# Optimization experiments

Measured on AMD Instinct MI355X. Metric: run time of the kernel, lower is better.

## Reference

```python
import jax, jax.numpy as jnp
import numpy as np

D_MODEL = 512
N_LAYERS = 4
VOCAB = 256
SEQ = 2048
BATCH = 8
EPS = 1e-5


def _ln(x, g, b):
    mu = jnp.mean(x, axis=-1, keepdims=True)
    var = jnp.mean(jnp.square(x - mu), axis=-1, keepdims=True)
    return (x - mu) * jax.lax.rsqrt(var + EPS) * g + b


def setup_inputs() -> dict:
    key = jax.random.key(0)
    ks = jax.random.split(key, 16)
    d, dff = D_MODEL, 4 * D_MODEL
    s = 0.02
    inp = {
        "tokens": jax.random.randint(ks[0], (BATCH, SEQ), 0, VOCAB, dtype=jnp.int64),
        "emb": jax.random.normal(ks[1], (VOCAB, d), jnp.float32) * s,
        "W_upd": jax.random.normal(ks[2], (d, d), jnp.float32) * s,
        "b_upd": jnp.zeros((d,), jnp.float32),
        "W_f": jax.random.normal(ks[3], (d, d), jnp.float32) * s,
        "b_f": jnp.zeros((d,), jnp.float32),
        "decay_param": jnp.zeros((1,), jnp.float32),
        "norm_g": jnp.ones((d,), jnp.float32),
        "norm_b": jnp.zeros((d,), jnp.float32),
        "cms_ln_g": jnp.ones((N_LAYERS, d), jnp.float32),
        "cms_ln_b": jnp.zeros((N_LAYERS, d), jnp.float32),
        "cms_W1": jax.random.normal(ks[4], (N_LAYERS, d, dff), jnp.float32) * s,
        "cms_b1": jnp.zeros((N_LAYERS, dff), jnp.float32),
        "cms_W2": jax.random.normal(ks[5], (N_LAYERS, dff, d), jnp.float32) * s,
        "cms_b2": jnp.zeros((N_LAYERS, d), jnp.float32),
        "head_W": jax.random.normal(ks[6], (d, VOCAB), jnp.float32) * s,
        "head_b": jnp.zeros((VOCAB,), jnp.float32),
    }
    return inp


def _fast_memory(x, mask, W_upd, b_upd, W_f, b_f, decay_param):
    # x: (B,S,d), mask: (B,S) float
    decay = jax.nn.sigmoid(decay_param[0])
    u = jnp.einsum("bsd,de->bse", x, W_upd) + b_upd  # precompute updates
    u_t = jnp.swapaxes(u, 0, 1)                        # (S,B,d)
    m_t = jnp.swapaxes(mask, 0, 1)[..., None]          # (S,B,1)

    def step(mem, inp):
        u_i, msk = inp
        new = decay * mem + u_i
        mem = msk * new + (1.0 - msk) * mem
        return mem, mem

    mem0 = jnp.zeros((x.shape[0], x.shape[2]), x.dtype)
    _, mems = jax.lax.scan(step, mem0, (u_t, m_t))     # (S,B,d)
    mems = jnp.swapaxes(mems, 0, 1)                    # (B,S,d)
    return jnp.einsum("bsd,de->bse", mems, W_f) + b_f


def reference(tokens, emb, W_upd, b_upd, W_f, b_f, decay_param, norm_g, norm_b,
              cms_ln_g, cms_ln_b, cms_W1, cms_b1, cms_W2, cms_b2, head_W, head_b):
    mask = (tokens != 0).astype(emb.dtype)
    x = emb[tokens]                                    # (B,S,d)
    x = x + _fast_memory(x, mask, W_upd, b_upd, W_f, b_f, decay_param)
    x = _ln(x, norm_g, norm_b)
    for i in range(N_LAYERS):
        h = _ln(x, cms_ln_g[i], cms_ln_b[i])
        h = jax.nn.gelu(jnp.einsum("bsd,df->bsf", h, cms_W1[i]) + cms_b1[i], approximate=False)
        h = jnp.einsum("bsf,fd->bsd", h, cms_W2[i]) + cms_b2[i]
        x = x + h
    return jnp.einsum("bsd,dv->bsv", x, head_W) + head_b
```

## Files before the change

### kernel.cpp

```cpp
#include <hip/hip_runtime.h>
#include <hip/hip_bf16.h>
#include <math.h>

#define D_MODEL 512
#define N_LAYERS 4
#define SEQ 2048
#define BATCH 8
#define M_TOT (BATCH * SEQ)
#define DFF 2048
#define HEAD_V 256
#define SC 32
#define NC (SEQ / SC)

typedef __hip_bfloat16 bf16;
typedef __bf16 bf16x8 __attribute__((ext_vector_type(8)));
typedef float f32x4 __attribute__((ext_vector_type(4)));

__device__ __forceinline__ unsigned short bfbits(float x) {
    bf16 h = __float2bfloat16(x);
    return *(unsigned short*)&h;
}
__device__ __forceinline__ unsigned int pk(float a, float b) {
    return (unsigned int)bfbits(a) | ((unsigned int)bfbits(b) << 16);
}

__device__ __forceinline__ float gelu_f(float x) {
    float t2 = 1.5957691216f * (x + 0.044715f * x * x * x);
    float e = __expf(t2);
    return x - x * __builtin_amdgcn_rcpf(e + 1.0f);
}

__global__ void convT_kernel(const float* __restrict__ W, bf16* __restrict__ WT,
                             int R, int C, size_t wstride, size_t tstride) {
    W += (size_t)blockIdx.z * wstride;
    WT += (size_t)blockIdx.z * tstride;
    __shared__ float t[32][33];
    int r0 = blockIdx.x * 32, c0 = blockIdx.y * 32;
    int tx = threadIdx.x, ty = threadIdx.y;
    #pragma unroll
    for (int i = 0; i < 32; i += 8)
        t[ty + i][tx] = W[(size_t)(r0 + ty + i) * C + c0 + tx];
    __syncthreads();
    #pragma unroll
    for (int i = 0; i < 32; i += 8)
        WT[(size_t)(c0 + ty + i) * R + r0 + tx] = __float2bfloat16(t[tx][ty + i]);
}

__global__ void embed_kernel(const int* __restrict__ tokens,
                             const float* __restrict__ emb,
                             float* __restrict__ xf, bf16* __restrict__ xb) {
    int row = blockIdx.x, t = threadIdx.x;
    int tok = tokens[row];
    float4 v = ((const float4*)(emb + (size_t)tok * D_MODEL))[t];
    ((float4*)(xf + (size_t)row * D_MODEL))[t] = v;
    uint2 st; st.x = pk(v.x, v.y); st.y = pk(v.z, v.w);
    ((uint2*)(xb + (size_t)row * D_MODEL))[t] = st;
}

__global__ void scanA_kernel(bf16* __restrict__ u, const int* __restrict__ tokens,
                             const float* __restrict__ decayp,
                             float* __restrict__ L, float* __restrict__ P) {
    int idx = blockIdx.x;
    int dblk = idx & 1;
    int c = (idx >> 1) & (NC - 1);
    int b = idx >> 7;
    int d = dblk * 256 + threadIdx.x;
    float decay = 1.0f / (1.0f + __expf(-decayp[0]));
    const int* tok = tokens + (size_t)b * SEQ + c * SC;
    bf16* up = u + ((size_t)b * SEQ + (size_t)c * SC) * D_MODEL + d;
    float mem = 0.0f;
    #pragma unroll 4
    for (int s = 0; s < SC; ++s) {
        float ui = __bfloat162float(up[(size_t)s * D_MODEL]);
        bool m = (tok[s] != 0);
        mem = (m ? decay : 1.0f) * mem + (m ? ui : 0.0f);
        up[(size_t)s * D_MODEL] = __float2bfloat16(mem);
    }
    L[((size_t)b * NC + c) * D_MODEL + d] = mem;
    if (threadIdx.x == 0 && dblk == 0) {
        int cnt = 0;
        for (int s = 0; s < SC; ++s) cnt += (tok[s] != 0);
        P[b * NC + c] = __powf(decay, (float)cnt);
    }
}

__global__ void scanB_kernel(const float* __restrict__ L, const float* __restrict__ P,
                             float* __restrict__ Mc) {
    int b = blockIdx.x >> 1;
    int d = (blockIdx.x & 1) * 256 + threadIdx.x;
    float carry = 0.0f;
    for (int c = 0; c < NC; ++c) {
        size_t off = ((size_t)b * NC + c) * D_MODEL + d;
        Mc[off] = carry;
        carry = P[b * NC + c] * carry + L[off];
    }
}

__global__ void scanC_kernel(bf16* __restrict__ u, const int* __restrict__ tokens,
                             const float* __restrict__ decayp,
                             const float* __restrict__ Mc) {
    int idx = blockIdx.x;
    int dblk = idx & 1;
    int c = (idx >> 1) & (NC - 1);
    int b = idx >> 7;
    if (c == 0) return;
    int d = dblk * 256 + threadIdx.x;
    float decay = 1.0f / (1.0f + __expf(-decayp[0]));
    const int* tok = tokens + (size_t)b * SEQ + c * SC;
    bf16* up = u + ((size_t)b * SEQ + (size_t)c * SC) * D_MODEL + d;
    float carry = Mc[((size_t)b * NC + c) * D_MODEL + d];
    float coeff = 1.0f;
    #pragma unroll 4
    for (int s = 0; s < SC; ++s) {
        bool m = (tok[s] != 0);
        coeff *= (m ? decay : 1.0f);
        float local = __bfloat162float(up[(size_t)s * D_MODEL]);
        up[(size_t)s * D_MODEL] = __float2bfloat16(local + carry * coeff);
    }
}

__device__ __forceinline__ void ln_body(const float* __restrict__ in,
                                        float* __restrict__ outf,
                                        bf16* __restrict__ outb,
                                        const float* __restrict__ g,
                                        const float* __restrict__ b,
                                        int WF, int WB) {
    int w = threadIdx.x >> 6, lane = threadIdx.x & 63;
    int row = blockIdx.x * 4 + w;
    const float4* ip = (const float4*)(in + (size_t)row * D_MODEL);
    float4 v0 = ip[lane * 2], v1 = ip[lane * 2 + 1];
    float s1 = v0.x + v0.y + v0.z + v0.w + v1.x + v1.y + v1.z + v1.w;
    float s2 = v0.x * v0.x + v0.y * v0.y + v0.z * v0.z + v0.w * v0.w +
               v1.x * v1.x + v1.y * v1.y + v1.z * v1.z + v1.w * v1.w;
    #pragma unroll
    for (int off = 32; off; off >>= 1) {
        s1 += __shfl_xor(s1, off);
        s2 += __shfl_xor(s2, off);
    }
    float mu = s1 * (1.0f / D_MODEL);
    float var = s2 * (1.0f / D_MODEL) - mu * mu;
    float rstd = rsqrtf(var + 1e-5f);
    const float4* g4 = (const float4*)g;
    const float4* b4 = (const float4*)b;
    float4 g0 = g4[lane * 2], g1 = g4[lane * 2 + 1];
    float4 b0 = b4[lane * 2], b1 = b4[lane * 2 + 1];
    float4 o0, o1;
    o0.x = (v0.x - mu) * rstd * g0.x + b0.x;
    o0.y = (v0.y - mu) * rstd * g0.y + b0.y;
    o0.z = (v0.z - mu) * rstd * g0.z + b0.z;
    o0.w = (v0.w - mu) * rstd * g0.w + b0.w;
    o1.x = (v1.x - mu) * rstd * g1.x + b1.x;
    o1.y = (v1.y - mu) * rstd * g1.y + b1.y;
    o1.z = (v1.z - mu) * rstd * g1.z + b1.z;
    o1.w = (v1.w - mu) * rstd * g1.w + b1.w;
    if (WF) {
        float4* op = (float4*)(outf + (size_t)row * D_MODEL);
        op[lane * 2] = o0; op[lane * 2 + 1] = o1;
    }
    if (WB) {
        uint4 st;
        st.x = pk(o0.x, o0.y); st.y = pk(o0.z, o0.w);
        st.z = pk(o1.x, o1.y); st.w = pk(o1.z, o1.w);
        ((uint4*)(outb + (size_t)row * D_MODEL))[lane] = st;
    }
}

__global__ void ln_f32_kernel(const float* __restrict__ in, float* __restrict__ outf,
                              const float* __restrict__ g, const float* __restrict__ b) {
    ln_body(in, outf, nullptr, g, b, 1, 0);
}
__global__ void ln_b16_kernel(const float* __restrict__ in, bf16* __restrict__ outb,
                              const float* __restrict__ g, const float* __restrict__ b) {
    ln_body(in, nullptr, outb, g, b, 0, 1);
}

#define STAGE(s, k0)                                                          \
    do {                                                                      \
        _Pragma("unroll")                                                     \
        for (int it = 0; it < 4; ++it) {                                      \
            int c = tid + it * 256;                                           \
            int p = c * 16;                                                   \
            int l = p ^ (((p >> 7) & 7) << 4);                                \
            __builtin_amdgcn_global_load_lds(                                 \
                A + (size_t)(m0 + (l >> 6)) * K + (k0) + ((l & 63) >> 1),     \
                smem + (s) * ABYTES + (c & ~63) * 16, 16, 0, 0);              \
        }                                                                     \
        _Pragma("unroll")                                                     \
        for (int it = 0; it < LB; ++it) {                                     \
            int c = tid + it * 256;                                           \
            int p = c * 16;                                                   \
            int l = p ^ (((p >> 7) & 7) << 4);                                \
            __builtin_amdgcn_global_load_lds(                                 \
                BT + (size_t)(n0 + (l >> 6)) * K + (k0) + ((l & 63) >> 1),    \
                smem + 2 * ABYTES + (s) * BBYTES + (c & ~63) * 16, 16, 0, 0); \
        }                                                                     \
    } while (0)

template <int BN, int GELU, int RES, int OBF>
__device__ __forceinline__ void gemm_body(char* smem,
                          const bf16* __restrict__ A, const bf16* __restrict__ BT,
                          const float* __restrict__ bias, const float* __restrict__ R,
                          float* __restrict__ Cf, bf16* __restrict__ Cb,
                          int N, int K) {
    constexpr int NJ = BN / 32;
    constexpr int MI = 8;
    constexpr int LB = BN / 64;
    constexpr int ABYTES = 256 * 32 * 2;
    constexpr int BBYTES = BN * 32 * 2;
    constexpr int ST = 16 * NJ + 4;
    const int tid = threadIdx.x;
    const int lane = tid & 63;
    const int w = tid >> 6, wr = w >> 1, wc = w & 1;
    const int lm = lane & 15, lk = lane >> 4;
    const int sw = ((lm >> 1) & 7) << 4;
    const int m0 = blockIdx.x * 256, n0 = blockIdx.y * BN;

    f32x4 acc[MI][NJ] = {};

    const int nt = K / 32;
    STAGE(0, 0);
    asm volatile("s_waitcnt vmcnt(0)" ::: "memory");
    __builtin_amdgcn_s_barrier();
    __builtin_amdgcn_sched_barrier(0);
    int cur = 0;
    for (int t = 0; t < nt; ++t) {
        if (t + 1 < nt) STAGE(cur ^ 1, (t + 1) * 32);
        const char* Asc = smem + cur * ABYTES;
        const char* Bsc = smem + 2 * ABYTES + cur * BBYTES;
        bf16x8 fa[MI], fb[NJ];
        #pragma unroll
        for (int i = 0; i < MI; ++i) {
            int la = (wr * 128 + i * 16 + lm) * 64 + lk * 16;
            fa[i] = *(const bf16x8*)(Asc + (la ^ sw));
        }
        #pragma unroll
        for (int j = 0; j < NJ; ++j) {
            int lb = (wc * (BN / 2) + j * 16 + lm) * 64 + lk * 16;
            fb[j] = *(const bf16x8*)(Bsc + (lb ^ sw));
        }
        #pragma unroll
        for (int i = 0; i < MI; ++i)
            #pragma unroll
            for (int j = 0; j < NJ; ++j)
                acc[i][j] = __builtin_amdgcn_mfma_f32_16x16x32_bf16(fa[i], fb[j], acc[i][j], 0, 0, 0);
        asm volatile("s_waitcnt vmcnt(0)" ::: "memory");
        __builtin_amdgcn_s_barrier();
        __builtin_amdgcn_sched_barrier(0);
        cur ^= 1;
    }

    float* ep = (float*)smem + w * 16 * ST;
    const int r2 = lane >> 2;
    const int q = lane & 3;
    constexpr int CW = 16 * NJ;
    const int gc0 = n0 + wc * CW + q * 4 * NJ;
    #pragma unroll
    for (int i = 0; i < MI; ++i) {
        #pragma unroll
        for (int j = 0; j < NJ; ++j)
            #pragma unroll
            for (int r = 0; r < 4; ++r)
                ep[(lk * 4 + r) * ST + j * 16 + lm] = acc[i][j][r];
        int grow = m0 + wr * 128 + i * 16 + r2;
        float4 fx[NJ];
        #pragma unroll
        for (int v = 0; v < NJ; ++v)
            fx[v] = *(const float4*)&ep[r2 * ST + q * 4 * NJ + v * 4];
        #pragma unroll
        for (int v = 0; v < NJ; ++v) {
            float4 bb = *(const float4*)(bias + gc0 + v * 4);
            fx[v].x += bb.x; fx[v].y += bb.y; fx[v].z += bb.z; fx[v].w += bb.w;
            if (GELU) {
                fx[v].x = gelu_f(fx[v].x);
                fx[v].y = gelu_f(fx[v].y);
                fx[v].z = gelu_f(fx[v].z);
                fx[v].w = gelu_f(fx[v].w);
            }
            if (RES) {
                float4 rr = *(const float4*)(R + (size_t)grow * N + gc0 + v * 4);
                fx[v].x += rr.x; fx[v].y += rr.y; fx[v].z += rr.z; fx[v].w += rr.w;
            }
        }
        if (OBF == 0 || OBF == 2) {
            #pragma unroll
            for (int v = 0; v < NJ; ++v)
                *(float4*)(Cf + (size_t)grow * N + gc0 + v * 4) = fx[v];
        }
        if (OBF >= 1) {
            #pragma unroll
            for (int v = 0; v < NJ; v += 2) {
                uint4 st;
                st.x = pk(fx[v].x, fx[v].y);
                st.y = pk(fx[v].z, fx[v].w);
                st.z = pk(fx[v + 1].x, fx[v + 1].y);
                st.w = pk(fx[v + 1].z, fx[v + 1].w);
                *(uint4*)(Cb + (size_t)grow * N + gc0 + v * 4) = st;
            }
        }
    }
}

#define DEF_GEMM(name, BN, GELU, RES, OBF)                                    \
__launch_bounds__(256, 2) __global__ void name(                               \
        const bf16* __restrict__ A, const bf16* __restrict__ BT,              \
        const float* __restrict__ bias, const float* __restrict__ R,          \
        float* __restrict__ Cf, bf16* __restrict__ Cb, int N, int K) {        \
    __shared__ char smem[2 * 16384 + 2 * (BN) * 64];                          \
    gemm_body<BN, GELU, RES, OBF>(smem, A, BT, bias, R, Cf, Cb, N, K);        \
}

DEF_GEMM(gemm_u,       128, 0, 0, 1)
DEF_GEMM(gemm_res,     128, 0, 1, 0)
DEF_GEMM(gemm_gelu,    128, 1, 0, 1)
DEF_GEMM(gemm_resboth, 128, 0, 1, 2)
DEF_GEMM(gemm64_plain,  64, 0, 0, 0)

extern "C" void kernel_launch(void* const* d_in, const int* in_sizes, int n_in,
                              void* d_out, int out_size, void* d_ws, size_t ws_size,
                              hipStream_t stream) {
    const int*   tokens = (const int*)d_in[0];
    const float* emb    = (const float*)d_in[1];
    const float* W_upd  = (const float*)d_in[2];
    const float* b_upd  = (const float*)d_in[3];
    const float* W_f    = (const float*)d_in[4];
    const float* b_f    = (const float*)d_in[5];
    const float* decayp = (const float*)d_in[6];
    const float* norm_g = (const float*)d_in[7];
    const float* norm_b = (const float*)d_in[8];
    const float* cms_g  = (const float*)d_in[9];
    const float* cms_b  = (const float*)d_in[10];
    const float* cW1    = (const float*)d_in[11];
    const float* cb1    = (const float*)d_in[12];
    const float* cW2    = (const float*)d_in[13];
    const float* cb2    = (const float*)d_in[14];
    const float* head_W = (const float*)d_in[15];
    const float* head_b = (const float*)d_in[16];
    float* out = (float*)d_out;

    const int M = M_TOT, D = D_MODEL, F = DFF, V = HEAD_V;

    float* xf = (float*)d_ws;
    bf16*  lnb = (bf16*)((char*)d_ws + (size_t)M * D * 4);
    bf16*  wb  = (bf16*)((char*)lnb + (size_t)M * D * 2);
    const size_t WB_ELEMS = 9043968;
    char* dyn = (char*)wb + WB_ELEMS * 2;
    size_t used = (size_t)(dyn - (char*)d_ws);
    size_t avail = ws_size > used ? ws_size - used : 0;
    int MC = 4096;
    if (avail >= (size_t)16384 * F * 2) MC = 16384;
    else if (avail >= (size_t)8192 * F * 2) MC = 8192;
    bf16* ub = (bf16*)dyn;
    bf16* hb = (bf16*)dyn;

    float* scanL = out;
    float* scanM = out + (size_t)BATCH * NC * D;
    float* scanP = scanM + (size_t)BATCH * NC * D;

    bf16* WupdT = wb;
    bf16* WfT   = wb + 262144;
    bf16* W1T   = wb + 524288;
    bf16* W2T   = wb + 4718592;
    bf16* HWT   = wb + 8912896;

    dim3 tb(32, 8);
    convT_kernel<<<dim3(16, 16, 2), tb, 0, stream>>>(W_upd, WupdT, D, D,
                                                     (size_t)(W_f - W_upd), 262144);
    convT_kernel<<<dim3(16, 64, N_LAYERS), tb, 0, stream>>>(cW1, W1T, D, F,
                                                            (size_t)D * F, 1048576);
    convT_kernel<<<dim3(64, 16, N_LAYERS), tb, 0, stream>>>(cW2, W2T, F, D,
                                                            (size_t)F * D, 1048576);
    convT_kernel<<<dim3(16, 8, 1), tb, 0, stream>>>(head_W, HWT, D, V, 0, 0);

    embed_kernel<<<M, 128, 0, stream>>>(tokens, emb, xf, lnb);

    gemm_u<<<dim3(M / 256, D / 128), 256, 0, stream>>>(
        lnb, WupdT, b_upd, nullptr, nullptr, ub, D, D);
    scanA_kernel<<<BATCH * NC * 2, 256, 0, stream>>>(ub, tokens, decayp, scanL, scanP);
    scanB_kernel<<<BATCH * 2, 256, 0, stream>>>(scanL, scanP, scanM);
    scanC_kernel<<<BATCH * NC * 2, 256, 0, stream>>>(ub, tokens, decayp, scanM);
    gemm_res<<<dim3(M / 256, D / 128), 256, 0, stream>>>(
        ub, WfT, b_f, xf, xf, nullptr, D, D);
    ln_f32_kernel<<<M / 4, 256, 0, stream>>>(xf, xf, norm_g, norm_b);

    for (int l = 0; l < N_LAYERS; ++l) {
        ln_b16_kernel<<<M / 4, 256, 0, stream>>>(xf, lnb,
                                                 cms_g + (size_t)l * D,
                                                 cms_b + (size_t)l * D);
        bool last = (l == N_LAYERS - 1);
        for (int mc = 0; mc < M; mc += MC) {
            gemm_gelu<<<dim3(MC / 256, F / 128), 256, 0, stream>>>(
                lnb + (size_t)mc * D, W1T + (size_t)l * 1048576,
                cb1 + (size_t)l * F, nullptr, nullptr, hb, F, D);
            if (last)
                gemm_resboth<<<dim3(MC / 256, D / 128), 256, 0, stream>>>(
                    hb, W2T + (size_t)l * 1048576, cb2 + (size_t)l * D,
                    xf + (size_t)mc * D, xf + (size_t)mc * D,
                    lnb + (size_t)mc * D, D, F);
            else
                gemm_res<<<dim3(MC / 256, D / 128), 256, 0, stream>>>(
                    hb, W2T + (size_t)l * 1048576, cb2 + (size_t)l * D,
                    xf + (size_t)mc * D, xf + (size_t)mc * D, nullptr, D, F);
        }
    }

    gemm64_plain<<<dim3(M / 256, V / 64), 256, 0, stream>>>(
        lnb, HWT, head_b, nullptr, out, nullptr, V, D);
}
```

Baseline: 607.5 us.

## Rewrite GEMM mainloop with 512 threads, BK=64 triple-buffered LDS pipeline

```diff
diff --git a/kernel.cpp b/kernel.cpp
--- a/kernel.cpp
+++ b/kernel.cpp
@@ -174,100 +174,147 @@
     ln_body(in, nullptr, outb, g, b, 0, 1);
 }
 
-#define STAGE(s, k0)                                                          \
+#define BUFB 49152
+
+#define STAGE_A(buf, k0)                                                      \
     do {                                                                      \
         _Pragma("unroll")                                                     \
         for (int it = 0; it < 4; ++it) {                                      \
-            int c = tid + it * 256;                                           \
-            int p = c * 16;                                                   \
-            int l = p ^ (((p >> 7) & 7) << 4);                                \
+            int c = tid + it * 512;                                           \
+            int r = c >> 3, s = c & 7;                                        \
             __builtin_amdgcn_global_load_lds(                                 \
-                A + (size_t)(m0 + (l >> 6)) * K + (k0) + ((l & 63) >> 1),     \
-                smem + (s) * ABYTES + (c & ~63) * 16, 16, 0, 0);              \
+                A + (size_t)(m0 + r) * K + (k0) + 8 * (s ^ (r & 7)),          \
+                smem + (buf) * BUFB + c * 16, 16, 0, 0);                      \
         }                                                                     \
+    } while (0)
+
+#define STAGE_B(buf, k0)                                                      \
+    do {                                                                      \
         _Pragma("unroll")                                                     \
-        for (int it = 0; it < LB; ++it) {                                     \
-            int c = tid + it * 256;                                           \
-            int p = c * 16;                                                   \
-            int l = p ^ (((p >> 7) & 7) << 4);                                \
+        for (int it = 0; it < 2; ++it) {                                      \
+            int c = tid + it * 512;                                           \
+            int r = c >> 3, s = c & 7;                                        \
             __builtin_amdgcn_global_load_lds(                                 \
-                BT + (size_t)(n0 + (l >> 6)) * K + (k0) + ((l & 63) >> 1),    \
-                smem + 2 * ABYTES + (s) * BBYTES + (c & ~63) * 16, 16, 0, 0); \
+                BT + (size_t)(n0 + r) * K + (k0) + 8 * (s ^ (r & 7)),         \
+                smem + (buf) * BUFB + 32768 + c * 16, 16, 0, 0);              \
         }                                                                     \
     } while (0)
 
-template <int BN, int GELU, int RES, int OBF>
+#define LOAD_FA(IH, KS)                                                       \
+    do {                                                                      \
+        fa0 = *(const bf16x8*)(Ab + (wr * 128 + ((IH) * 4 + 0) * 16 + lm) * 128 + (((KS) * 64 + lk * 16) ^ swz)); \
+        fa1 = *(const bf16x8*)(Ab + (wr * 128 + ((IH) * 4 + 1) * 16 + lm) * 128 + (((KS) * 64 + lk * 16) ^ swz)); \
+        fa2 = *(const bf16x8*)(Ab + (wr * 128 + ((IH) * 4 + 2) * 16 + lm) * 128 + (((KS) * 64 + lk * 16) ^ swz)); \
+        fa3 = *(const bf16x8*)(Ab + (wr * 128 + ((IH) * 4 + 3) * 16 + lm) * 128 + (((KS) * 64 + lk * 16) ^ swz)); \
+    } while (0)
+
+#define LOAD_FB(KS)                                                           \
+    do {                                                                      \
+        fb0 = *(const bf16x8*)(Bb + (wc * 32 + 0 + lm) * 128 + (((KS) * 64 + lk * 16) ^ swz)); \
+        fb1 = *(const bf16x8*)(Bb + (wc * 32 + 16 + lm) * 128 + (((KS) * 64 + lk * 16) ^ swz)); \
+    } while (0)
+
+#define MFMA8(B0)                                                             \
+    do {                                                                      \
+        acc[(B0) + 0][0] = __builtin_amdgcn_mfma_f32_16x16x32_bf16(fa0, fb0, acc[(B0) + 0][0], 0, 0, 0); \
+        acc[(B0) + 0][1] = __builtin_amdgcn_mfma_f32_16x16x32_bf16(fa0, fb1, acc[(B0) + 0][1], 0, 0, 0); \
+        acc[(B0) + 1][0] = __builtin_amdgcn_mfma_f32_16x16x32_bf16(fa1, fb0, acc[(B0) + 1][0], 0, 0, 0); \
+        acc[(B0) + 1][1] = __builtin_amdgcn_mfma_f32_16x16x32_bf16(fa1, fb1, acc[(B0) + 1][1], 0, 0, 0); \
+        acc[(B0) + 2][0] = __builtin_amdgcn_mfma_f32_16x16x32_bf16(fa2, fb0, acc[(B0) + 2][0], 0, 0, 0); \
+        acc[(B0) + 2][1] = __builtin_amdgcn_mfma_f32_16x16x32_bf16(fa2, fb1, acc[(B0) + 2][1], 0, 0, 0); \
+        acc[(B0) + 3][0] = __builtin_amdgcn_mfma_f32_16x16x32_bf16(fa3, fb0, acc[(B0) + 3][0], 0, 0, 0); \
+        acc[(B0) + 3][1] = __builtin_amdgcn_mfma_f32_16x16x32_bf16(fa3, fb1, acc[(B0) + 3][1], 0, 0, 0); \
+    } while (0)
+
+#define PHASE_PRE                                                             \
+    do {                                                                      \
+        __builtin_amdgcn_s_barrier();                                         \
+        asm volatile("s_waitcnt lgkmcnt(0)" ::: "memory");                    \
+        __builtin_amdgcn_sched_barrier(0);                                    \
+        __builtin_amdgcn_s_setprio(1);                                        \
+    } while (0)
+
+#define PHASE_POST                                                            \
+    do {                                                                      \
+        __builtin_amdgcn_s_setprio(0);                                        \
+        __builtin_amdgcn_s_barrier();                                         \
+    } while (0)
+
+template <int GELU, int RES, int OBF>
 __device__ __forceinline__ void gemm_body(char* smem,
                           const bf16* __restrict__ A, const bf16* __restrict__ BT,
                           const float* __restrict__ bias, const float* __restrict__ R,
                           float* __restrict__ Cf, bf16* __restrict__ Cb,
                           int N, int K) {
-    constexpr int NJ = BN / 32;
-    constexpr int MI = 8;
-    constexpr int LB = BN / 64;
-    constexpr int ABYTES = 256 * 32 * 2;
-    constexpr int BBYTES = BN * 32 * 2;
-    constexpr int ST = 16 * NJ + 4;
+    constexpr int ST = 36;
     const int tid = threadIdx.x;
     const int lane = tid & 63;
-    const int w = tid >> 6, wr = w >> 1, wc = w & 1;
+    const int w = tid >> 6;
+    const int wr = w >> 2, wc = w & 3;
     const int lm = lane & 15, lk = lane >> 4;
-    const int sw = ((lm >> 1) & 7) << 4;
-    const int m0 = blockIdx.x * 256, n0 = blockIdx.y * BN;
-
-    f32x4 acc[MI][NJ] = {};
-
-    const int nt = K / 32;
-    STAGE(0, 0);
-    asm volatile("s_waitcnt vmcnt(0)" ::: "memory");
+    const int swz = (lm & 7) << 4;
+    const int m0 = blockIdx.x * 256, n0 = blockIdx.y * 128;
+
+    f32x4 acc[8][2] = {};
+    const int nt = K / 64;
+
+    STAGE_A(0, 0); STAGE_B(0, 0);
+    STAGE_A(1, 64); STAGE_B(1, 64);
+    asm volatile("s_waitcnt vmcnt(6)" ::: "memory");
     __builtin_amdgcn_s_barrier();
     __builtin_amdgcn_sched_barrier(0);
+
     int cur = 0;
     for (int t = 0; t < nt; ++t) {
-        if (t + 1 < nt) STAGE(cur ^ 1, (t + 1) * 32);
-        const char* Asc = smem + cur * ABYTES;
-        const char* Bsc = smem + 2 * ABYTES + cur * BBYTES;
-        bf16x8 fa[MI], fb[NJ];
-        #pragma unroll
-        for (int i = 0; i < MI; ++i) {
-            int la = (wr * 128 + i * 16 + lm) * 64 + lk * 16;
-            fa[i] = *(const bf16x8*)(Asc + (la ^ sw));
-        }
-        #pragma unroll
-        for (int j = 0; j < NJ; ++j) {
-            int lb = (wc * (BN / 2) + j * 16 + lm) * 64 + lk * 16;
-            fb[j] = *(const bf16x8*)(Bsc + (lb ^ sw));
-        }
-        #pragma unroll
-        for (int i = 0; i < MI; ++i)
-            #pragma unroll
-            for (int j = 0; j < NJ; ++j)
-                acc[i][j] = __builtin_amdgcn_mfma_f32_16x16x32_bf16(fa[i], fb[j], acc[i][j], 0, 0, 0);
-        asm volatile("s_waitcnt vmcnt(0)" ::: "memory");
+        const char* Ab = smem + cur * BUFB;
+        const char* Bb = Ab + 32768;
+        int nb = cur + 2; if (nb >= 3) nb -= 3;
+        bf16x8 fa0, fa1, fa2, fa3, fb0, fb1;
+        LOAD_FB(0);
+        LOAD_FA(0, 0);
+        if (t + 2 < nt) STAGE_A(nb, (t + 2) * 64);
+        PHASE_PRE;
+        MFMA8(0);
+        PHASE_POST;
+        LOAD_FA(1, 0);
+        if (t + 2 < nt) STAGE_B(nb, (t + 2) * 64);
+        PHASE_PRE;
+        MFMA8(4);
+        PHASE_POST;
+        LOAD_FB(1);
+        LOAD_FA(0, 1);
+        PHASE_PRE;
+        MFMA8(0);
+        PHASE_POST;
+        LOAD_FA(1, 1);
+        PHASE_PRE;
+        MFMA8(4);
+        __builtin_amdgcn_s_setprio(0);
+        if (t + 2 < nt) asm volatile("s_waitcnt vmcnt(6)" ::: "memory");
+        else            asm volatile("s_waitcnt vmcnt(0)" ::: "memory");
         __builtin_amdgcn_s_barrier();
         __builtin_amdgcn_sched_barrier(0);
-        cur ^= 1;
+        cur = (cur == 2) ? 0 : cur + 1;
     }
 
     float* ep = (float*)smem + w * 16 * ST;
     const int r2 = lane >> 2;
     const int q = lane & 3;
-    constexpr int CW = 16 * NJ;
-    const int gc0 = n0 + wc * CW + q * 4 * NJ;
+    const int gc0 = n0 + wc * 32 + q * 8;
     #pragma unroll
-    for (int i = 0; i < MI; ++i) {
+    for (int i = 0; i < 8; ++i) {
         #pragma unroll
-        for (int j = 0; j < NJ; ++j)
+        for (int j = 0; j < 2; ++j)
             #pragma unroll
             for (int r = 0; r < 4; ++r)
                 ep[(lk * 4 + r) * ST + j * 16 + lm] = acc[i][j][r];
         int grow = m0 + wr * 128 + i * 16 + r2;
-        float4 fx[NJ];
+        float4 fx[2];
         #pragma unroll
-        for (int v = 0; v < NJ; ++v)
-            fx[v] = *(const float4*)&ep[r2 * ST + q * 4 * NJ + v * 4];
+        for (int v = 0; v < 2; ++v)
+            fx[v] = *(const float4*)&ep[r2 * ST + q * 8 + v * 4];
         #pragma unroll
-        for (int v = 0; v < NJ; ++v) {
+        for (int v = 0; v < 2; ++v) {
             float4 bb = *(const float4*)(bias + gc0 + v * 4);
             fx[v].x += bb.x; fx[v].y += bb.y; fx[v].z += bb.z; fx[v].w += bb.w;
             if (GELU) {
@@ -283,37 +330,34 @@
         }
         if (OBF == 0 || OBF == 2) {
             #pragma unroll
-            for (int v = 0; v < NJ; ++v)
+            for (int v = 0; v < 2; ++v)
                 *(float4*)(Cf + (size_t)grow * N + gc0 + v * 4) = fx[v];
         }
         if (OBF >= 1) {
-            #pragma unroll
-            for (int v = 0; v < NJ; v += 2) {
-                uint4 st;
-                st.x = pk(fx[v].x, fx[v].y);
-                st.y = pk(fx[v].z, fx[v].w);
-                st.z = pk(fx[v + 1].x, fx[v + 1].y);
-                st.w = pk(fx[v + 1].z, fx[v + 1].w);
-                *(uint4*)(Cb + (size_t)grow * N + gc0 + v * 4) = st;
-            }
+            uint4 st;
+            st.x = pk(fx[0].x, fx[0].y);
+            st.y = pk(fx[0].z, fx[0].w);
+            st.z = pk(fx[1].x, fx[1].y);
+            st.w = pk(fx[1].z, fx[1].w);
+            *(uint4*)(Cb + (size_t)grow * N + gc0) = st;
         }
     }
 }
 
-#define DEF_GEMM(name, BN, GELU, RES, OBF)                                    \
-__launch_bounds__(256, 2) __global__ void name(                               \
+#define DEF_GEMM(name, GELU, RES, OBF)                                        \
+__launch_bounds__(512) __global__ void name(                                  \
         const bf16* __restrict__ A, const bf16* __restrict__ BT,              \
         const float* __restrict__ bias, const float* __restrict__ R,          \
         float* __restrict__ Cf, bf16* __restrict__ Cb, int N, int K) {        \
-    __shared__ char smem[2 * 16384 + 2 * (BN) * 64];                          \
-    gemm_body<BN, GELU, RES, OBF>(smem, A, BT, bias, R, Cf, Cb, N, K);        \
-}
-
-DEF_GEMM(gemm_u,       128, 0, 0, 1)
-DEF_GEMM(gemm_res,     128, 0, 1, 0)
-DEF_GEMM(gemm_gelu,    128, 1, 0, 1)
-DEF_GEMM(gemm_resboth, 128, 0, 1, 2)
-DEF_GEMM(gemm64_plain,  64, 0, 0, 0)
+    __shared__ char smem[3 * BUFB];                                           \
+    gemm_body<GELU, RES, OBF>(smem, A, BT, bias, R, Cf, Cb, N, K);            \
+}
+
+DEF_GEMM(gemm_u,       0, 0, 1)
+DEF_GEMM(gemm_res,     0, 1, 0)
+DEF_GEMM(gemm_gelu,    1, 0, 1)
+DEF_GEMM(gemm_resboth, 0, 1, 2)
+DEF_GEMM(gemm_plain,   0, 0, 0)
 
 extern "C" void kernel_launch(void* const* d_in, const int* in_sizes, int n_in,
                               void* d_out, int out_size, void* d_ws, size_t ws_size,
@@ -373,12 +417,12 @@
 
     embed_kernel<<<M, 128, 0, stream>>>(tokens, emb, xf, lnb);
 
-    gemm_u<<<dim3(M / 256, D / 128), 256, 0, stream>>>(
+    gemm_u<<<dim3(M / 256, D / 128), 512, 0, stream>>>(
         lnb, WupdT, b_upd, nullptr, nullptr, ub, D, D);
     scanA_kernel<<<BATCH * NC * 2, 256, 0, stream>>>(ub, tokens, decayp, scanL, scanP);
     scanB_kernel<<<BATCH * 2, 256, 0, stream>>>(scanL, scanP, scanM);
     scanC_kernel<<<BATCH * NC * 2, 256, 0, stream>>>(ub, tokens, decayp, scanM);
-    gemm_res<<<dim3(M / 256, D / 128), 256, 0, stream>>>(
+    gemm_res<<<dim3(M / 256, D / 128), 512, 0, stream>>>(
         ub, WfT, b_f, xf, xf, nullptr, D, D);
     ln_f32_kernel<<<M / 4, 256, 0, stream>>>(xf, xf, norm_g, norm_b);
 
@@ -388,21 +432,21 @@
                                                  cms_b + (size_t)l * D);
         bool last = (l == N_LAYERS - 1);
         for (int mc = 0; mc < M; mc += MC) {
-            gemm_gelu<<<dim3(MC / 256, F / 128), 256, 0, stream>>>(
+            gemm_gelu<<<dim3(MC / 256, F / 128), 512, 0, stream>>>(
                 lnb + (size_t)mc * D, W1T + (size_t)l * 1048576,
                 cb1 + (size_t)l * F, nullptr, nullptr, hb, F, D);
             if (last)
-                gemm_resboth<<<dim3(MC / 256, D / 128), 256, 0, stream>>>(
+                gemm_resboth<<<dim3(MC / 256, D / 128), 512, 0, stream>>>(
                     hb, W2T + (size_t)l * 1048576, cb2 + (size_t)l * D,
                     xf + (size_t)mc * D, xf + (size_t)mc * D,
                     lnb + (size_t)mc * D, D, F);
             else
-                gemm_res<<<dim3(MC / 256, D / 128), 256, 0, stream>>>(
+                gemm_res<<<dim3(MC / 256, D / 128), 512, 0, stream>>>(
                     hb, W2T + (size_t)l * 1048576, cb2 + (size_t)l * D,
                     xf + (size_t)mc * D, xf + (size_t)mc * D, nullptr, D, F);
         }
     }
 
-    gemm64_plain<<<dim3(M / 256, V / 64), 256, 0, stream>>>(
+    gemm_plain<<<dim3(M / 256, V / 128), 512, 0, stream>>>(
         lnb, HWT, head_b, nullptr, out, nullptr, V, D);
 }
```

New measurement: 554.9 us. -8.7%, faster.

## Restructure GEMM to 512-thread blocks with BK=64 tiles and vmcnt-based pipelining

Applied to the files above, without the earlier changes.

```diff
diff --git a/kernel.cpp b/kernel.cpp
--- a/kernel.cpp
+++ b/kernel.cpp
@@ -174,100 +174,109 @@
     ln_body(in, nullptr, outb, g, b, 0, 1);
 }
 
-#define STAGE(s, k0)                                                          \
+#define STAGE(buf, k0)                                                        \
     do {                                                                      \
         _Pragma("unroll")                                                     \
-        for (int it = 0; it < 4; ++it) {                                      \
-            int c = tid + it * 256;                                           \
-            int p = c * 16;                                                   \
-            int l = p ^ (((p >> 7) & 7) << 4);                                \
+        for (int it = 0; it < AL; ++it) {                                     \
+            int cc = tid + it * 512;                                          \
+            int rr = cc >> 3, ss = cc & 7;                                    \
             __builtin_amdgcn_global_load_lds(                                 \
-                A + (size_t)(m0 + (l >> 6)) * K + (k0) + ((l & 63) >> 1),     \
-                smem + (s) * ABYTES + (c & ~63) * 16, 16, 0, 0);              \
+                A + (size_t)(m0 + rr) * K + (k0) + 8 * (ss ^ (rr & 7)),       \
+                smem + (buf) * TILEB + cc * 16, 16, 0, 0);                    \
         }                                                                     \
         _Pragma("unroll")                                                     \
-        for (int it = 0; it < LB; ++it) {                                     \
-            int c = tid + it * 256;                                           \
-            int p = c * 16;                                                   \
-            int l = p ^ (((p >> 7) & 7) << 4);                                \
+        for (int it = 0; it < 4; ++it) {                                      \
+            int cc = tid + it * 512;                                          \
+            int rr = cc >> 3, ss = cc & 7;                                    \
             __builtin_amdgcn_global_load_lds(                                 \
-                BT + (size_t)(n0 + (l >> 6)) * K + (k0) + ((l & 63) >> 1),    \
-                smem + 2 * ABYTES + (s) * BBYTES + (c & ~63) * 16, 16, 0, 0); \
+                BT + (size_t)(n0 + rr) * K + (k0) + 8 * (ss ^ (rr & 7)),      \
+                smem + (buf) * TILEB + BM * 128 + cc * 16, 16, 0, 0);         \
         }                                                                     \
     } while (0)
 
-template <int BN, int GELU, int RES, int OBF>
+template <int WM, int GELU, int RES, int OBF>
 __device__ __forceinline__ void gemm_body(char* smem,
                           const bf16* __restrict__ A, const bf16* __restrict__ BT,
                           const float* __restrict__ bias, const float* __restrict__ R,
                           float* __restrict__ Cf, bf16* __restrict__ Cb,
                           int N, int K) {
-    constexpr int NJ = BN / 32;
-    constexpr int MI = 8;
-    constexpr int LB = BN / 64;
-    constexpr int ABYTES = 256 * 32 * 2;
-    constexpr int BBYTES = BN * 32 * 2;
-    constexpr int ST = 16 * NJ + 4;
+    constexpr int BM = 2 * WM;
+    constexpr int MI = WM / 16;
+    constexpr int AL = BM / 64;
+    constexpr int TILEB = (BM + 256) * 128;
+    constexpr int ST = 68;
     const int tid = threadIdx.x;
     const int lane = tid & 63;
-    const int w = tid >> 6, wr = w >> 1, wc = w & 1;
+    const int w = tid >> 6;
+    const int wr = w >> 2, wc = w & 3;
     const int lm = lane & 15, lk = lane >> 4;
-    const int sw = ((lm >> 1) & 7) << 4;
-    const int m0 = blockIdx.x * 256, n0 = blockIdx.y * BN;
-
-    f32x4 acc[MI][NJ] = {};
-
-    const int nt = K / 32;
+    const int swz = (lm & 7) << 4;
+    const int m0 = blockIdx.x * BM, n0 = blockIdx.y * 256;
+
+    f32x4 acc[MI][4] = {};
+    const int nt = K >> 6;
+
     STAGE(0, 0);
-    asm volatile("s_waitcnt vmcnt(0)" ::: "memory");
-    __builtin_amdgcn_s_barrier();
-    __builtin_amdgcn_sched_barrier(0);
     int cur = 0;
     for (int t = 0; t < nt; ++t) {
-        if (t + 1 < nt) STAGE(cur ^ 1, (t + 1) * 32);
-        const char* Asc = smem + cur * ABYTES;
-        const char* Bsc = smem + 2 * ABYTES + cur * BBYTES;
-        bf16x8 fa[MI], fb[NJ];
-        #pragma unroll
-        for (int i = 0; i < MI; ++i) {
-            int la = (wr * 128 + i * 16 + lm) * 64 + lk * 16;
-            fa[i] = *(const bf16x8*)(Asc + (la ^ sw));
-        }
-        #pragma unroll
-        for (int j = 0; j < NJ; ++j) {
-            int lb = (wc * (BN / 2) + j * 16 + lm) * 64 + lk * 16;
-            fb[j] = *(const bf16x8*)(Bsc + (lb ^ sw));
-        }
-        #pragma unroll
-        for (int i = 0; i < MI; ++i)
-            #pragma unroll
-            for (int j = 0; j < NJ; ++j)
-                acc[i][j] = __builtin_amdgcn_mfma_f32_16x16x32_bf16(fa[i], fb[j], acc[i][j], 0, 0, 0);
-        asm volatile("s_waitcnt vmcnt(0)" ::: "memory");
+        if (t + 1 < nt) {
+            STAGE(cur ^ 1, (t + 1) * 64);
+            if constexpr (AL == 4) asm volatile("s_waitcnt vmcnt(8)" ::: "memory");
+            else                   asm volatile("s_waitcnt vmcnt(6)" ::: "memory");
+        } else {
+            asm volatile("s_waitcnt vmcnt(0)" ::: "memory");
+        }
         __builtin_amdgcn_s_barrier();
         __builtin_amdgcn_sched_barrier(0);
+        const char* Ab = smem + cur * TILEB;
+        const char* Bb = Ab + BM * 128;
+        #pragma unroll
+        for (int ks = 0; ks < 2; ++ks) {
+            bf16x8 fb[4];
+            #pragma unroll
+            for (int nf = 0; nf < 4; ++nf)
+                fb[nf] = *(const bf16x8*)(Bb + (wc * 64 + nf * 16 + lm) * 128 +
+                                          ((ks * 64 + lk * 16) ^ swz));
+            #pragma unroll
+            for (int mh = 0; mh < MI / 4; ++mh) {
+                bf16x8 fa[4];
+                #pragma unroll
+                for (int mf = 0; mf < 4; ++mf)
+                    fa[mf] = *(const bf16x8*)(Ab + (wr * WM + (mh * 4 + mf) * 16 + lm) * 128 +
+                                              ((ks * 64 + lk * 16) ^ swz));
+                __builtin_amdgcn_s_setprio(1);
+                #pragma unroll
+                for (int mf = 0; mf < 4; ++mf)
+                    #pragma unroll
+                    for (int nf = 0; nf < 4; ++nf)
+                        acc[mh * 4 + mf][nf] = __builtin_amdgcn_mfma_f32_16x16x32_bf16(
+                            fa[mf], fb[nf], acc[mh * 4 + mf][nf], 0, 0, 0);
+                __builtin_amdgcn_s_setprio(0);
+            }
+        }
+        __builtin_amdgcn_s_barrier();
         cur ^= 1;
     }
+    __syncthreads();
 
     float* ep = (float*)smem + w * 16 * ST;
     const int r2 = lane >> 2;
     const int q = lane & 3;
-    constexpr int CW = 16 * NJ;
-    const int gc0 = n0 + wc * CW + q * 4 * NJ;
+    const int gc0 = n0 + wc * 64 + q * 16;
     #pragma unroll
     for (int i = 0; i < MI; ++i) {
         #pragma unroll
-        for (int j = 0; j < NJ; ++j)
+        for (int nf = 0; nf < 4; ++nf)
             #pragma unroll
             for (int r = 0; r < 4; ++r)
-                ep[(lk * 4 + r) * ST + j * 16 + lm] = acc[i][j][r];
-        int grow = m0 + wr * 128 + i * 16 + r2;
-        float4 fx[NJ];
+                ep[(lk * 4 + r) * ST + nf * 16 + lm] = acc[i][nf][r];
+        int grow = m0 + wr * WM + i * 16 + r2;
+        float4 fx[4];
         #pragma unroll
-        for (int v = 0; v < NJ; ++v)
-            fx[v] = *(const float4*)&ep[r2 * ST + q * 4 * NJ + v * 4];
+        for (int v = 0; v < 4; ++v)
+            fx[v] = *(const float4*)&ep[r2 * ST + q * 16 + v * 4];
         #pragma unroll
-        for (int v = 0; v < NJ; ++v) {
+        for (int v = 0; v < 4; ++v) {
             float4 bb = *(const float4*)(bias + gc0 + v * 4);
             fx[v].x += bb.x; fx[v].y += bb.y; fx[v].z += bb.z; fx[v].w += bb.w;
             if (GELU) {
@@ -283,37 +292,35 @@
         }
         if (OBF == 0 || OBF == 2) {
             #pragma unroll
-            for (int v = 0; v < NJ; ++v)
+            for (int v = 0; v < 4; ++v)
                 *(float4*)(Cf + (size_t)grow * N + gc0 + v * 4) = fx[v];
         }
         if (OBF >= 1) {
-            #pragma unroll
-            for (int v = 0; v < NJ; v += 2) {
-                uint4 st;
-                st.x = pk(fx[v].x, fx[v].y);
-                st.y = pk(fx[v].z, fx[v].w);
-                st.z = pk(fx[v + 1].x, fx[v + 1].y);
-                st.w = pk(fx[v + 1].z, fx[v + 1].w);
-                *(uint4*)(Cb + (size_t)grow * N + gc0 + v * 4) = st;
-            }
-        }
-    }
-}
-
-#define DEF_GEMM(name, BN, GELU, RES, OBF)                                    \
-__launch_bounds__(256, 2) __global__ void name(                               \
+            uint4 s1, s2;
+            s1.x = pk(fx[0].x, fx[0].y); s1.y = pk(fx[0].z, fx[0].w);
+            s1.z = pk(fx[1].x, fx[1].y); s1.w = pk(fx[1].z, fx[1].w);
+            s2.x = pk(fx[2].x, fx[2].y); s2.y = pk(fx[2].z, fx[2].w);
+            s2.z = pk(fx[3].x, fx[3].y); s2.w = pk(fx[3].z, fx[3].w);
+            *(uint4*)(Cb + (size_t)grow * N + gc0) = s1;
+            *(uint4*)(Cb + (size_t)grow * N + gc0 + 8) = s2;
+        }
+    }
+}
+
+#define DEF_GEMM(name, WM, GELU, RES, OBF)                                    \
+__launch_bounds__(512) __global__ void name(                                  \
         const bf16* __restrict__ A, const bf16* __restrict__ BT,              \
         const float* __restrict__ bias, const float* __restrict__ R,          \
         float* __restrict__ Cf, bf16* __restrict__ Cb, int N, int K) {        \
-    __shared__ char smem[2 * 16384 + 2 * (BN) * 64];                          \
-    gemm_body<BN, GELU, RES, OBF>(smem, A, BT, bias, R, Cf, Cb, N, K);        \
-}
-
-DEF_GEMM(gemm_u,       128, 0, 0, 1)
-DEF_GEMM(gemm_res,     128, 0, 1, 0)
+    __shared__ char smem[2 * ((2 * (WM)) + 256) * 128];                       \
+    gemm_body<WM, GELU, RES, OBF>(smem, A, BT, bias, R, Cf, Cb, N, K);        \
+}
+
 DEF_GEMM(gemm_gelu,    128, 1, 0, 1)
-DEF_GEMM(gemm_resboth, 128, 0, 1, 2)
-DEF_GEMM(gemm64_plain,  64, 0, 0, 0)
+DEF_GEMM(gemm_u,        64, 0, 0, 1)
+DEF_GEMM(gemm_res,      64, 0, 1, 0)
+DEF_GEMM(gemm_resboth,  64, 0, 1, 2)
+DEF_GEMM(gemm_plain,    64, 0, 0, 0)
 
 extern "C" void kernel_launch(void* const* d_in, const int* in_sizes, int n_in,
                               void* d_out, int out_size, void* d_ws, size_t ws_size,
@@ -373,12 +380,12 @@
 
     embed_kernel<<<M, 128, 0, stream>>>(tokens, emb, xf, lnb);
 
-    gemm_u<<<dim3(M / 256, D / 128), 256, 0, stream>>>(
+    gemm_u<<<dim3(M / 128, D / 256), 512, 0, stream>>>(
         lnb, WupdT, b_upd, nullptr, nullptr, ub, D, D);
     scanA_kernel<<<BATCH * NC * 2, 256, 0, stream>>>(ub, tokens, decayp, scanL, scanP);
     scanB_kernel<<<BATCH * 2, 256, 0, stream>>>(scanL, scanP, scanM);
     scanC_kernel<<<BATCH * NC * 2, 256, 0, stream>>>(ub, tokens, decayp, scanM);
-    gemm_res<<<dim3(M / 256, D / 128), 256, 0, stream>>>(
+    gemm_res<<<dim3(M / 128, D / 256), 512, 0, stream>>>(
         ub, WfT, b_f, xf, xf, nullptr, D, D);
     ln_f32_kernel<<<M / 4, 256, 0, stream>>>(xf, xf, norm_g, norm_b);
 
@@ -388,21 +395,21 @@
                                                  cms_b + (size_t)l * D);
         bool last = (l == N_LAYERS - 1);
         for (int mc = 0; mc < M; mc += MC) {
-            gemm_gelu<<<dim3(MC / 256, F / 128), 256, 0, stream>>>(
+            gemm_gelu<<<dim3(MC / 256, F / 256), 512, 0, stream>>>(
                 lnb + (size_t)mc * D, W1T + (size_t)l * 1048576,
                 cb1 + (size_t)l * F, nullptr, nullptr, hb, F, D);
             if (last)
-                gemm_resboth<<<dim3(MC / 256, D / 128), 256, 0, stream>>>(
+                gemm_resboth<<<dim3(MC / 128, D / 256), 512, 0, stream>>>(
                     hb, W2T + (size_t)l * 1048576, cb2 + (size_t)l * D,
                     xf + (size_t)mc * D, xf + (size_t)mc * D,
                     lnb + (size_t)mc * D, D, F);
             else
-                gemm_res<<<dim3(MC / 256, D / 128), 256, 0, stream>>>(
+                gemm_res<<<dim3(MC / 128, D / 256), 512, 0, stream>>>(
                     hb, W2T + (size_t)l * 1048576, cb2 + (size_t)l * D,
                     xf + (size_t)mc * D, xf + (size_t)mc * D, nullptr, D, F);
         }
     }
 
-    gemm64_plain<<<dim3(M / 256, V / 64), 256, 0, stream>>>(
+    gemm_plain<<<dim3(M / 128, V / 256), 512, 0, stream>>>(
         lnb, HWT, head_b, nullptr, out, nullptr, V, D);
 }
```

Measured after the change: 539.1 us. -11.2%, faster.
